# Kernel tuning notes

Hardware: AMD Instinct MI355X
Metric: run time of the kernel (lower is better)

Reference implementation:

```python
import jax, jax.numpy as jnp
import numpy as np

G, P_IN, P_OUT, C_Q = 4, 32, 128, 256
STRIDES = [4, 8, 16, 32]
TAU = 2.0
EPS = 1e-5


def _ln(x, axes):
    m = jnp.mean(x, axes, keepdims=True)
    v = jnp.var(x, axes, keepdims=True)
    return (x - m) * jax.lax.rsqrt(v + EPS)


def _grid_sample(value, pts):
    # torch F.grid_sample, bilinear, padding_mode='zeros', align_corners=False
    # value: [Bg, C, H, W], pts: [Bg, Q, P, 2] in [-1, 1] (x, y order)
    Bg, C, H, W = value.shape
    x = (pts[..., 0] + 1.0) * (W * 0.5) - 0.5
    y = (pts[..., 1] + 1.0) * (H * 0.5) - 0.5
    x0 = jnp.floor(x)
    y0 = jnp.floor(y)
    flat = value.reshape(Bg, C, H * W)
    Q, P = pts.shape[1], pts.shape[2]

    def corner(xf, yf, w):
        valid = (xf >= 0) & (xf <= W - 1) & (yf >= 0) & (yf <= H - 1)
        xi = jnp.clip(xf, 0, W - 1).astype(jnp.int32)
        yi = jnp.clip(yf, 0, H - 1).astype(jnp.int32)
        idx = (yi * W + xi).reshape(Bg, 1, Q * P)
        g = jnp.take_along_axis(flat, idx, axis=2).reshape(Bg, C, Q, P)
        return g * (w * valid)[:, None]

    out = (corner(x0, y0, (x0 + 1 - x) * (y0 + 1 - y))
           + corner(x0 + 1, y0, (x - x0) * (y0 + 1 - y))
           + corner(x0, y0 + 1, (x0 + 1 - x) * (y - y0))
           + corner(x0 + 1, y0 + 1, (x - x0) * (y - y0)))
    return out  # [Bg, C, Q, P]


def setup_inputs() -> dict:
    key = jax.random.key(0)
    ks = jax.random.split(key, 12)
    B, N = 2, 300
    sizes = [(200, 336), (100, 168), (50, 84), (25, 42)]
    xs = [jax.random.normal(ks[i], (B, 256, h, w), jnp.float32) for i, (h, w) in enumerate(sizes)]
    query_feat = jax.random.normal(ks[4], (B, N, C_Q), jnp.float32)
    u = jax.random.uniform(ks[5], (B, N, 4), jnp.float32)
    # xyzr roi: center x in [0,1344], y in [0,800], z (log2 scale) in [3,6], r in [-1,1]
    query_roi = jnp.stack([u[..., 0] * 1344.0, u[..., 1] * 800.0,
                           3.0 + 3.0 * u[..., 2], 2.0 * u[..., 3] - 1.0], axis=-1)
    w_off = jax.random.normal(ks[6], (C_Q, G * P_IN * 3), jnp.float32) * 0.01
    b = jax.random.uniform(ks[7], (G, P_IN, 3), jnp.float32, minval=-0.5, maxval=0.5)
    b_off = b.at[:, :, 2].set(-1.0).reshape(-1)
    cg = 256 // G
    total = G * (cg * cg + P_IN * P_OUT)
    pg_w = jax.random.normal(ks[8], (C_Q, total), jnp.float32) * 0.02
    pg_b = jax.random.normal(ks[9], (total,), jnp.float32) * 0.02
    op_w = jax.random.normal(ks[10], (G * P_OUT * cg, C_Q), jnp.float32) * 0.02
    op_b = jnp.zeros((C_Q,), jnp.float32)
    ln_g = jnp.ones((C_Q,), jnp.float32)
    ln_b = jnp.zeros((C_Q,), jnp.float32)
    return dict(x0=xs[0], x1=xs[1], x2=xs[2], x3=xs[3], query_feat=query_feat,
                query_roi=query_roi, w_off=w_off, b_off=b_off, pg_w=pg_w, pg_b=pg_b,
                op_w=op_w, op_b=op_b, ln_g=ln_g, ln_b=ln_b)


def reference(x0, x1, x2, x3, query_feat, query_roi, w_off, b_off,
              pg_w, pg_b, op_w, op_b, ln_g, ln_b):
    xs = [x0, x1, x2, x3]
    B, N, _ = query_feat.shape
    Cf = x0.shape[1]
    Cg = Cf // G
    L = len(xs)

    # ---- make_sample_points ----
    off = (query_feat @ w_off + b_off).reshape(B, N, G * P_IN, 3)
    xy = query_roi[..., :2]
    z = query_roi[..., 2:3]
    r = query_roi[..., 3:4]
    roi_wh = (2.0 ** z) * jnp.concatenate([2.0 ** (-0.5 * r), 2.0 ** (0.5 * r)], axis=-1)
    samp_xy = xy[:, :, None, :] + off[..., :2] * roi_wh[:, :, None, :]   # [B,N,GP,2]
    samp_lvl = z[:, :, None, :] + off[..., 2:3]                          # [B,N,GP,1]

    # ---- level weights: softmax(-(lvl-3 - l)^2 / tau) ----
    grid = jnp.arange(L, dtype=samp_lvl.dtype)
    lw = jax.nn.softmax(-(((samp_lvl - 3.0) - grid) ** 2) / TAU, axis=-1)  # [B,N,GP,L]

    # ---- multiscale sampling ----
    out = jnp.zeros((B * G, Cg, N, P_IN), x0.dtype)
    for i, (v, s) in enumerate(zip(xs, STRIDES)):
        H, W = v.shape[2], v.shape[3]
        size = jnp.array([W * s, H * s], samp_xy.dtype)
        pts = samp_xy / size * 2.0 - 1.0
        pts = pts.reshape(B, N, G, P_IN, 2).transpose(0, 2, 1, 3, 4).reshape(B * G, N, P_IN, 2)
        val = v.reshape(B * G, Cg, H, W)
        w = lw[..., i].reshape(B, N, G, P_IN).transpose(0, 2, 1, 3).reshape(B * G, 1, N, P_IN)
        out = out + _grid_sample(val, pts) * w
    sampled = out.reshape(B, G, Cg, N, P_IN).transpose(0, 3, 1, 4, 2)  # [B,N,G,P_IN,Cg]

    # ---- AdaptiveMixing ----
    params = (query_feat @ pg_w + pg_b).reshape(B, N, G, -1)
    M = params[..., :Cg * Cg].reshape(B, N, G, Cg, Cg)
    S = params[..., Cg * Cg:].reshape(B, N, G, P_OUT, P_IN)
    h = jnp.einsum('bngpc,bngcd->bngpd', sampled, M)
    h = jax.nn.relu(_ln(h, (-2, -1)))
    h = jnp.einsum('bngop,bngpc->bngoc', S, h)
    h = jax.nn.relu(_ln(h, (-2, -1)))
    q = query_feat + h.reshape(B, N, -1) @ op_w + op_b

    # ---- final LayerNorm (learned) ----
    return _ln(q, (-1,)) * ln_g + ln_b
```

## Files before the change

### kernel.cpp

```cpp
#include <hip/hip_runtime.h>
#include <cstdint>
#include <cstddef>

typedef __bf16 bf16;
typedef _Float16 f16;
typedef __attribute__((ext_vector_type(8))) __bf16 bf16x8;
typedef __attribute__((ext_vector_type(4))) __bf16 bf16x4;
typedef __attribute__((ext_vector_type(4))) float f32x4;
typedef __attribute__((ext_vector_type(2))) float f32x2;
typedef __attribute__((ext_vector_type(2))) uint32_t u32x2;

#define DINL __device__ __forceinline__

DINL float wred(float v) {
#pragma unroll
  for (int m = 32; m; m >>= 1) v += __shfl_xor(v, m, 64);
  return v;
}

DINL int swz(int r) { return ((r ^ (r >> 2)) & 7) << 4; }

__global__ void k_zero(float* __restrict__ p) {
  p[blockIdx.x * 256 + threadIdx.x] = 0.f;
}

__global__ void k_coords(const float* __restrict__ qf, const float* __restrict__ roi,
                         const float* __restrict__ w_off, const float* __restrict__ b_off,
                         float* __restrict__ coords) {
  int bn = blockIdx.x;
  int t = threadIdx.x;
  __shared__ float qs[256];
  __shared__ float offs[384];
  if (t < 256) qs[t] = qf[(size_t)bn * 256 + t];
  __syncthreads();
  float acc = b_off[t];
  for (int k = 0; k < 256; k++) acc += qs[k] * w_off[k * 384 + t];
  offs[t] = acc;
  __syncthreads();
  if (t < 128) {
    float ox = offs[t * 3 + 0], oy = offs[t * 3 + 1], oz = offs[t * 3 + 2];
    float cx = roi[bn * 4 + 0], cy = roi[bn * 4 + 1];
    float z  = roi[bn * 4 + 2], rr = roi[bn * 4 + 3];
    float sx = cx + ox * exp2f(z - 0.5f * rr);
    float sy = cy + oy * exp2f(z + 0.5f * rr);
    float lvl = z + oz;
    float e[4], mx = -1e30f;
#pragma unroll
    for (int l = 0; l < 4; l++) {
      float d = lvl - 3.0f - (float)l;
      e[l] = -d * d * 0.5f;
      mx = fmaxf(mx, e[l]);
    }
    float s = 0.f;
#pragma unroll
    for (int l = 0; l < 4; l++) { e[l] = expf(e[l] - mx); s += e[l]; }
    float inv = 1.f / s;
    float* o = coords + ((size_t)bn * 128 + t) * 6;
    o[0] = sx; o[1] = sy;
#pragma unroll
    for (int l = 0; l < 4; l++) o[2 + l] = e[l] * inv;
  }
}

__global__ __launch_bounds__(256) void k_xpose(
    const float* __restrict__ x0, const float* __restrict__ x1,
    const float* __restrict__ x2, const float* __restrict__ x3,
    f16* __restrict__ xt, int bg0, size_t slab) {
  const int HWl[4]  = {67200, 16800, 4200, 1050};
  const int RB[4]   = {0, 67200, 84000, 88200};
  const float* xs[4] = {x0, x1, x2, x3};
  int bx = blockIdx.x;
  int l, t0;
  if (bx < 525)      { l = 0; t0 = 0; }
  else if (bx < 657) { l = 1; t0 = 525; }
  else if (bx < 690) { l = 2; t0 = 657; }
  else               { l = 3; t0 = 690; }
  int HW = HWl[l];
  int sp0 = (bx - t0) * 128;
  int bg = bg0 + blockIdx.z;
  int b = bg >> 2, g = bg & 3;
  const float* src = xs[l] + (size_t)(b * 256 + g * 64) * HW;
  __shared__ f16 tile[128 * 66];
  int tid = threadIdx.x;
  int lane = tid & 63, wv = tid >> 6;
  int sp = sp0 + lane * 2;
  if (sp < HW) {
#pragma unroll
    for (int j = 0; j < 16; j++) {
      int ch = wv * 16 + j;
      f32x2 v = *(const f32x2*)(src + (size_t)ch * HW + sp);
      tile[(lane * 2 + 0) * 66 + ch] = (f16)v[0];
      tile[(lane * 2 + 1) * 66 + ch] = (f16)v[1];
    }
  }
  __syncthreads();
  f16* dst = xt + slab * blockIdx.z + (size_t)(RB[l] + sp0) * 64;
  int c4 = tid & 15, srow = tid >> 4;
  const uint32_t* tp = (const uint32_t*)(&tile[0]);
#pragma unroll
  for (int it = 0; it < 8; it++) {
    int s = it * 16 + srow;
    if (sp0 + s < HW) {
      u32x2 pk;
      pk[0] = tp[s * 33 + c4 * 2];
      pk[1] = tp[s * 33 + c4 * 2 + 1];
      *(u32x2*)(dst + (size_t)s * 64 + c4 * 4) = pk;
    }
  }
}

__global__ __launch_bounds__(256) void k_sample2(
    const float* __restrict__ coords, const f16* __restrict__ xt,
    bf16* __restrict__ sampled, int bg0, size_t slab) {
  const int   Wl[4] = {336, 168, 84, 42};
  const int   Hl[4] = {200, 100, 50, 25};
  const int   RB[4] = {0, 67200, 84000, 88200};
  const float IS[4] = {0.25f, 0.125f, 0.0625f, 0.03125f};
  int bg = bg0 + blockIdx.z;
  int b = bg >> 2, g = bg & 3;
  int bn = b * 300 + blockIdx.x;
  const f16* xts = xt + slab * blockIdx.z;
  int c = threadIdx.x & 63, pp = threadIdx.x >> 6;
#pragma unroll
  for (int p8i = 0; p8i < 4; p8i++) {
    int p8 = blockIdx.y * 4 + p8i;
    int p = p8 * 4 + pp;
    const float* cd = coords + ((size_t)bn * 128 + g * 32 + p) * 6;
    float sx = cd[0], sy = cd[1];
    float acc = 0.f;
#pragma unroll
    for (int l = 0; l < 4; l++) {
      float wl = cd[2 + l];
      int W = Wl[l], H = Hl[l];
      float xf = sx * IS[l] - 0.5f;
      float yf = sy * IS[l] - 0.5f;
      float xx0 = floorf(xf), yy0 = floorf(yf);
      float fx = xf - xx0, fy = yf - yy0;
      int xi = (int)xx0, yi = (int)yy0;
      const f16* base = xts + (size_t)RB[l] * 64 + c;
      float v = 0.f;
      if (xi >= 0     && xi < W     && yi >= 0     && yi < H)
        v += (1.f - fx) * (1.f - fy) * (float)base[(size_t)(yi * W + xi) * 64];
      if (xi + 1 >= 0 && xi + 1 < W && yi >= 0     && yi < H)
        v += fx * (1.f - fy) * (float)base[(size_t)(yi * W + xi + 1) * 64];
      if (xi >= 0     && xi < W     && yi + 1 >= 0 && yi + 1 < H)
        v += (1.f - fx) * fy * (float)base[(size_t)((yi + 1) * W + xi) * 64];
      if (xi + 1 >= 0 && xi + 1 < W && yi + 1 >= 0 && yi + 1 < H)
        v += fx * fy * (float)base[(size_t)((yi + 1) * W + xi + 1) * 64];
      acc += wl * v;
    }
    sampled[(((size_t)bn * 4 + g) * 32 + p) * 64 + c] = (bf16)acc;
  }
}

__global__ __launch_bounds__(256) void k_params_mfma(
    const float* __restrict__ qf, const float* __restrict__ pg_w,
    const float* __restrict__ pg_b, bf16* __restrict__ pchunk,
    int m_off, int m_cnt) {
  __shared__ char sA[8192];
  __shared__ char sW[32768];
  const int tid = threadIdx.x;
  const int w = tid >> 6, l = tid & 63;
  const int lr = l & 15, lq = l >> 4;
  const int m0 = blockIdx.y * 64;
  const int n0 = blockIdx.x * 256;

  f32x4 acc[4][4];
#pragma unroll
  for (int i = 0; i < 4; i++)
#pragma unroll
    for (int j = 0; j < 4; j++) acc[i][j] = (f32x4)(0.f);

  for (int kt = 0; kt < 4; kt++) {
    const int kb = kt * 64;

#pragma unroll
    for (int i = 0; i < 2; i++) {
      int c = tid * 2 + i;
      int r = c >> 3, kc = c & 7;
      int gm = m0 + r; gm = (gm < m_cnt) ? gm : (m_cnt - 1);
      const float* src = qf + (size_t)(m_off + gm) * 256 + kb + kc * 8;
      f32x4 v0 = *(const f32x4*)src;
      f32x4 v1 = *(const f32x4*)(src + 4);
      bf16x8 t = {(bf16)v0[0], (bf16)v0[1], (bf16)v0[2], (bf16)v0[3],
                  (bf16)v1[0], (bf16)v1[1], (bf16)v1[2], (bf16)v1[3]};
      *(bf16x8*)(sA + r * 128 + ((kc << 4) ^ swz(r))) = t;
    }

#pragma unroll
    for (int i = 0; i < 4; i++) {
      int kblk = i * 4 + w;
      const float* src = pg_w + (size_t)(kb + kblk * 4) * 32768 + n0 + l * 4;
      f32x4 r0 = *(const f32x4*)(src);
      f32x4 r1 = *(const f32x4*)(src + 32768);
      f32x4 r2 = *(const f32x4*)(src + 65536);
      f32x4 r3 = *(const f32x4*)(src + 98304);
      int chv = (kblk >> 1) << 4;
      int sub = (kblk & 1) * 8;
#pragma unroll
      for (int j = 0; j < 4; j++) {
        int n = l * 4 + j;
        bf16x4 t = {(bf16)r0[j], (bf16)r1[j], (bf16)r2[j], (bf16)r3[j]};
        *(bf16x4*)(sW + n * 128 + (chv ^ swz(n)) + sub) = t;
      }
    }
    __syncthreads();

#pragma unroll
    for (int ks = 0; ks < 2; ks++) {
      bf16x8 a[4], b[4];
      int ch = (ks * 4 + lq) << 4;
#pragma unroll
      for (int i = 0; i < 4; i++) {
        int row = i * 16 + lr;
        a[i] = *(const bf16x8*)(sA + row * 128 + (ch ^ swz(row)));
      }
#pragma unroll
      for (int j = 0; j < 4; j++) {
        int nn = w * 64 + j * 16 + lr;
        b[j] = *(const bf16x8*)(sW + nn * 128 + (ch ^ swz(nn)));
      }
#pragma unroll
      for (int i = 0; i < 4; i++)
#pragma unroll
        for (int j = 0; j < 4; j++)
          acc[i][j] = __builtin_amdgcn_mfma_f32_16x16x32_bf16(a[i], b[j], acc[i][j], 0, 0, 0);
    }
    __syncthreads();
  }

#pragma unroll
  for (int i = 0; i < 4; i++) {
#pragma unroll
    for (int r = 0; r < 4; r++) {
      int m = m0 + i * 16 + lq * 4 + r;
      if (m < m_cnt) {
        bf16* dst = pchunk + (size_t)m * 32768 + n0 + w * 64 + lr;
#pragma unroll
        for (int j = 0; j < 4; j++) {
          int n = n0 + w * 64 + j * 16 + lr;
          dst[j * 16] = (bf16)(acc[i][j][r] + pg_b[n]);
        }
      }
    }
  }
}

__global__ __launch_bounds__(256) void k_mix_mfma(
    const bf16* __restrict__ sampled, bf16* __restrict__ params, int m_off) {
  int bnl = blockIdx.x, g = blockIdx.y;
  int tid = threadIdx.x;
  const int w = tid >> 6, l = tid & 63;
  const int lr = l & 15, lq = l >> 4;
  __shared__ char mt[8192];
  __shared__ alignas(16) bf16 h1t[64 * 40];
  __shared__ float red[8];
  const bf16* samp = sampled + ((size_t)(m_off + bnl) * 4 + g) * 2048;
  bf16* pr = params + (size_t)bnl * 32768 + (size_t)g * 8192;

  {
    int cblk = tid >> 4, dblk = tid & 15;
    const bf16* src = pr + cblk * 256 + dblk * 4;
    bf16x4 r0 = *(const bf16x4*)(src);
    bf16x4 r1 = *(const bf16x4*)(src + 64);
    bf16x4 r2 = *(const bf16x4*)(src + 128);
    bf16x4 r3 = *(const bf16x4*)(src + 192);
    int chv = (cblk >> 1) << 4, sub = (cblk & 1) * 8;
#pragma unroll
    for (int j = 0; j < 4; j++) {
      int d = dblk * 4 + j;
      bf16x4 t = {r0[j], r1[j], r2[j], r3[j]};
      *(bf16x4*)(mt + d * 128 + (chv ^ swz(d)) + sub) = t;
    }
  }
  __syncthreads();

  f32x4 acc1[2];
  acc1[0] = (f32x4)(0.f); acc1[1] = (f32x4)(0.f);
  const int dd = w * 16 + lr;
#pragma unroll
  for (int ks = 0; ks < 2; ks++) {
    bf16x8 b = *(const bf16x8*)(mt + dd * 128 + ((((ks << 2) | lq) << 4) ^ swz(dd)));
#pragma unroll
    for (int i = 0; i < 2; i++) {
      bf16x8 a = *(const bf16x8*)(samp + (i * 16 + lr) * 64 + ks * 32 + lq * 8);
      acc1[i] = __builtin_amdgcn_mfma_f32_16x16x32_bf16(a, b, acc1[i], 0, 0, 0);
    }
  }

  {
    float s = 0.f, ss = 0.f;
#pragma unroll
    for (int i = 0; i < 2; i++)
#pragma unroll
      for (int r = 0; r < 4; r++) { float v = acc1[i][r]; s += v; ss += v * v; }
    s = wred(s); ss = wred(ss);
    if (l == 0) { red[w] = s; red[4 + w] = ss; }
    __syncthreads();
    s = red[0] + red[1] + red[2] + red[3];
    ss = red[4] + red[5] + red[6] + red[7];
    float mean = s * (1.f / 2048.f);
    float var = ss * (1.f / 2048.f) - mean * mean;
    float rs = rsqrtf(fmaxf(var, 0.f) + 1e-5f);
#pragma unroll
    for (int i = 0; i < 2; i++)
#pragma unroll
      for (int r = 0; r < 4; r++) {
        float v = (acc1[i][r] - mean) * rs;
        v = v > 0.f ? v : 0.f;
        int p = i * 16 + lq * 4 + r;
        h1t[dd * 40 + p] = (bf16)v;
      }
  }
  __syncthreads();

  f32x4 acc2[2][4];
#pragma unroll
  for (int i = 0; i < 2; i++)
#pragma unroll
    for (int j = 0; j < 4; j++) acc2[i][j] = (f32x4)(0.f);
  bf16x8 b2[4];
#pragma unroll
  for (int j = 0; j < 4; j++)
    b2[j] = *(const bf16x8*)(&h1t[(j * 16 + lr) * 40 + lq * 8]);
#pragma unroll
  for (int i = 0; i < 2; i++) {
    int o = w * 32 + i * 16 + lr;
    bf16x8 a = *(const bf16x8*)(pr + 4096 + o * 32 + lq * 8);
#pragma unroll
    for (int j = 0; j < 4; j++)
      acc2[i][j] = __builtin_amdgcn_mfma_f32_16x16x32_bf16(a, b2[j], acc2[i][j], 0, 0, 0);
  }

  {
    float s = 0.f, ss = 0.f;
#pragma unroll
    for (int i = 0; i < 2; i++)
#pragma unroll
      for (int j = 0; j < 4; j++)
#pragma unroll
        for (int r = 0; r < 4; r++) { float v = acc2[i][j][r]; s += v; ss += v * v; }
    s = wred(s); ss = wred(ss);
    if (l == 0) { red[w] = s; red[4 + w] = ss; }
    __syncthreads();
    s = red[0] + red[1] + red[2] + red[3];
    ss = red[4] + red[5] + red[6] + red[7];
    float mean = s * (1.f / 8192.f);
    float var = ss * (1.f / 8192.f) - mean * mean;
    float rs = rsqrtf(fmaxf(var, 0.f) + 1e-5f);
#pragma unroll
    for (int i = 0; i < 2; i++)
#pragma unroll
      for (int r = 0; r < 4; r++) {
        int o = w * 32 + i * 16 + lq * 4 + r;
#pragma unroll
        for (int j = 0; j < 4; j++) {
          float v = (acc2[i][j][r] - mean) * rs;
          v = v > 0.f ? v : 0.f;
          pr[o * 64 + j * 16 + lr] = (bf16)v;
        }
      }
  }
}

__global__ __launch_bounds__(256) void k_final_mfma(
    const bf16* __restrict__ pchunk, const float* __restrict__ op_w,
    float* __restrict__ facc, int m_off, int m_cnt, int KT) {
  __shared__ char sA[8192];
  __shared__ char sW[32768];
  const int tid = threadIdx.x;
  const int w = tid >> 6, l = tid & 63;
  const int lr = l & 15, lq = l >> 4;
  const int m0 = blockIdx.y * 64;
  const int kb0 = blockIdx.x * (KT * 64);

  f32x4 acc[4][4];
#pragma unroll
  for (int i = 0; i < 4; i++)
#pragma unroll
    for (int j = 0; j < 4; j++) acc[i][j] = (f32x4)(0.f);

  for (int kt = 0; kt < KT; kt++) {
    const int kb = kb0 + kt * 64;

#pragma unroll
    for (int i = 0; i < 2; i++) {
      int c = tid * 2 + i;
      int r = c >> 3, kc = c & 7;
      int gm = m0 + r; gm = (gm < m_cnt) ? gm : (m_cnt - 1);
      f32x4 v = *(const f32x4*)(pchunk + (size_t)gm * 32768 + kb + kc * 8);
      *(f32x4*)(sA + r * 128 + ((kc << 4) ^ swz(r))) = v;
    }

#pragma unroll
    for (int i = 0; i < 4; i++) {
      int kblk = i * 4 + w;
      const float* src = op_w + (size_t)(kb + kblk * 4) * 256 + l * 4;
      f32x4 r0 = *(const f32x4*)(src);
      f32x4 r1 = *(const f32x4*)(src + 256);
      f32x4 r2 = *(const f32x4*)(src + 512);
      f32x4 r3 = *(const f32x4*)(src + 768);
      int chv = (kblk >> 1) << 4;
      int sub = (kblk & 1) * 8;
#pragma unroll
      for (int j = 0; j < 4; j++) {
        int n = l * 4 + j;
        bf16x4 t = {(bf16)r0[j], (bf16)r1[j], (bf16)r2[j], (bf16)r3[j]};
        *(bf16x4*)(sW + n * 128 + (chv ^ swz(n)) + sub) = t;
      }
    }
    __syncthreads();

#pragma unroll
    for (int ks = 0; ks < 2; ks++) {
      bf16x8 a[4], b[4];
      int ch = (ks * 4 + lq) << 4;
#pragma unroll
      for (int i = 0; i < 4; i++) {
        int row = i * 16 + lr;
        a[i] = *(const bf16x8*)(sA + row * 128 + (ch ^ swz(row)));
      }
#pragma unroll
      for (int j = 0; j < 4; j++) {
        int n = w * 64 + j * 16 + lr;
        b[j] = *(const bf16x8*)(sW + n * 128 + (ch ^ swz(n)));
      }
#pragma unroll
      for (int i = 0; i < 4; i++)
#pragma unroll
        for (int j = 0; j < 4; j++)
          acc[i][j] = __builtin_amdgcn_mfma_f32_16x16x32_bf16(a[i], b[j], acc[i][j], 0, 0, 0);
    }
    __syncthreads();
  }

#pragma unroll
  for (int i = 0; i < 4; i++) {
#pragma unroll
    for (int r = 0; r < 4; r++) {
      int m = m0 + i * 16 + lq * 4 + r;
      if (m < m_cnt) {
        float* dst = facc + (size_t)(m_off + m) * 256 + w * 64 + lr;
#pragma unroll
        for (int j = 0; j < 4; j++)
          atomicAdd(dst + j * 16, acc[i][j][r]);
      }
    }
  }
}

__global__ void k_ln(const float* __restrict__ accbuf, const float* __restrict__ qf,
                     const float* __restrict__ opb, const float* __restrict__ lng,
                     const float* __restrict__ lnb, float* __restrict__ out) {
  int bn = blockIdx.x, t = threadIdx.x;
  float v = accbuf[bn * 256 + t] + qf[(size_t)bn * 256 + t] + opb[t];
  __shared__ float red[8];
  float s = wred(v), ss = wred(v * v);
  int w = t >> 6;
  if ((t & 63) == 0) { red[w] = s; red[4 + w] = ss; }
  __syncthreads();
  s = red[0] + red[1] + red[2] + red[3];
  ss = red[4] + red[5] + red[6] + red[7];
  float mean = s * (1.f / 256.f);
  float var = ss * (1.f / 256.f) - mean * mean;
  float y = (v - mean) * rsqrtf(fmaxf(var, 0.f) + 1e-5f);
  out[(size_t)bn * 256 + t] = y * lng[t] + lnb[t];
}

extern "C" void kernel_launch(void* const* d_in, const int* in_sizes, int n_in,
                              void* d_out, int out_size, void* d_ws, size_t ws_size,
                              hipStream_t stream) {
  const float* x0    = (const float*)d_in[0];
  const float* x1    = (const float*)d_in[1];
  const float* x2    = (const float*)d_in[2];
  const float* x3    = (const float*)d_in[3];
  const float* qf    = (const float*)d_in[4];
  const float* roi   = (const float*)d_in[5];
  const float* w_off = (const float*)d_in[6];
  const float* b_off = (const float*)d_in[7];
  const float* pg_w  = (const float*)d_in[8];
  const float* pg_b  = (const float*)d_in[9];
  const float* op_w  = (const float*)d_in[10];
  const float* op_b  = (const float*)d_in[11];
  const float* ln_g  = (const float*)d_in[12];
  const float* ln_b  = (const float*)d_in[13];
  float* out = (float*)d_out;

  const size_t SLAB = 5712000;
  const size_t NEEDED_BIG  = 143001600ull;
  const size_t NEEDED_SMALL = 31948800ull;
  if (ws_size < NEEDED_SMALL) return;

  char* ws = (char*)d_ws;
  float* coords  = (float*)(ws + 0);
  bf16*  sampled = (bf16*)(ws + 1843200);
  float* facc    = (float*)(ws + 11673600);

  k_zero<<<600, 256, 0, stream>>>(facc);
  k_coords<<<600, 384, 0, stream>>>(qf, roi, w_off, b_off, coords);

  if (ws_size >= NEEDED_BIG) {
    bf16* params = (bf16*)(ws + 12288000);
    f16*  xt     = (f16*)(ws + 51609600);
    k_xpose<<<dim3(699, 1, 8), 256, 0, stream>>>(x0, x1, x2, x3, xt, 0, SLAB);
    k_sample2<<<dim3(300, 2, 8), 256, 0, stream>>>(coords, xt, sampled, 0, SLAB);
    k_params_mfma<<<dim3(128, 10), 256, 0, stream>>>(qf, pg_w, pg_b, params, 0, 600);
    k_mix_mfma<<<dim3(600, 4), 256, 0, stream>>>(sampled, params, 0);
    k_final_mfma<<<dim3(64, 10), 256, 0, stream>>>(params, op_w, facc, 0, 600, 8);
  } else {
    bf16* pchunk = (bf16*)(ws + 12288000);
    f16*  xt     = (f16*)(ws + 12288000);
    for (int bg = 0; bg < 8; bg++) {
      k_xpose<<<dim3(699, 1, 1), 256, 0, stream>>>(x0, x1, x2, x3, xt, bg, 0);
      k_sample2<<<dim3(300, 2, 1), 256, 0, stream>>>(coords, xt, sampled, bg, 0);
    }
    for (int chunk = 0; chunk < 2; chunk++) {
      int m_off = chunk * 300, m_cnt = 300;
      k_params_mfma<<<dim3(128, 5), 256, 0, stream>>>(qf, pg_w, pg_b, pchunk, m_off, m_cnt);
      k_mix_mfma<<<dim3(300, 4), 256, 0, stream>>>(sampled, pchunk, m_off);
      k_final_mfma<<<dim3(32, 5), 256, 0, stream>>>(pchunk, op_w, facc, m_off, m_cnt, 16);
    }
  }

  k_ln<<<600, 256, 0, stream>>>(facc, qf, op_b, ln_g, ln_b, out);
}
```

Before: 501.3 us.

## Fuse bilinear multiscale sampling into the adaptive mixing kernel

Removes the separate sampling kernel in the large-workspace path. Each mixing block now gathers its own 32x64 sampled tile straight from the transposed feature maps into swizzled shared memory and feeds it to the MFMA stage. This avoids writing the sampled tensor to global memory, reading it back, and one launch, at the cost of a longer per-block prologue. The transpose kernel also batches its global loads and LDS reads into registers before the stores, to raise memory-level parallelism.

Result: slower. 515.6 us (+2.9%).

```diff
diff --git a/kernel.cpp b/kernel.cpp
--- a/kernel.cpp
+++ b/kernel.cpp
@@ -19,6 +19,7 @@
 }
 
 DINL int swz(int r) { return ((r ^ (r >> 2)) & 7) << 4; }
+DINL int swzc(int r) { return (r ^ (r >> 2)) & 7; }
 
 __global__ void k_zero(float* __restrict__ p) {
   p[blockIdx.x * 256 + threadIdx.x] = 0.f;
@@ -85,26 +86,34 @@
   int lane = tid & 63, wv = tid >> 6;
   int sp = sp0 + lane * 2;
   if (sp < HW) {
+    f32x2 v[16];
+#pragma unroll
+    for (int j = 0; j < 16; j++)
+      v[j] = *(const f32x2*)(src + (size_t)(wv * 16 + j) * HW + sp);
 #pragma unroll
     for (int j = 0; j < 16; j++) {
       int ch = wv * 16 + j;
-      f32x2 v = *(const f32x2*)(src + (size_t)ch * HW + sp);
-      tile[(lane * 2 + 0) * 66 + ch] = (f16)v[0];
-      tile[(lane * 2 + 1) * 66 + ch] = (f16)v[1];
+      tile[(lane * 2 + 0) * 66 + ch] = (f16)v[j][0];
+      tile[(lane * 2 + 1) * 66 + ch] = (f16)v[j][1];
     }
   }
   __syncthreads();
   f16* dst = xt + slab * blockIdx.z + (size_t)(RB[l] + sp0) * 64;
   int c4 = tid & 15, srow = tid >> 4;
   const uint32_t* tp = (const uint32_t*)(&tile[0]);
+  uint32_t pk[16];
+#pragma unroll
+  for (int it = 0; it < 8; it++) {
+    int s = it * 16 + srow;
+    pk[it * 2 + 0] = tp[s * 33 + c4 * 2];
+    pk[it * 2 + 1] = tp[s * 33 + c4 * 2 + 1];
+  }
 #pragma unroll
   for (int it = 0; it < 8; it++) {
     int s = it * 16 + srow;
     if (sp0 + s < HW) {
-      u32x2 pk;
-      pk[0] = tp[s * 33 + c4 * 2];
-      pk[1] = tp[s * 33 + c4 * 2 + 1];
-      *(u32x2*)(dst + (size_t)s * 64 + c4 * 4) = pk;
+      u32x2 q; q[0] = pk[it * 2]; q[1] = pk[it * 2 + 1];
+      *(u32x2*)(dst + (size_t)s * 64 + c4 * 4) = q;
     }
   }
 }
@@ -246,6 +255,162 @@
   }
 }
 
+__global__ __launch_bounds__(256) void k_mix_fused(
+    const float* __restrict__ coords, const f16* __restrict__ xt,
+    bf16* __restrict__ params, size_t slab) {
+  const int   Wl[4] = {336, 168, 84, 42};
+  const int   Hl[4] = {200, 100, 50, 25};
+  const int   RB[4] = {0, 67200, 84000, 88200};
+  const float IS[4] = {0.25f, 0.125f, 0.0625f, 0.03125f};
+  int bn = blockIdx.x, g = blockIdx.y;
+  int b = (bn >= 300) ? 1 : 0;
+  int tid = threadIdx.x;
+  const int w = tid >> 6, l = tid & 63;
+  const int lr = l & 15, lq = l >> 4;
+  __shared__ char mt[8192];
+  __shared__ char samp_s[4096];
+  __shared__ alignas(16) bf16 h1t[64 * 40];
+  __shared__ float red[8];
+  bf16* pr = params + (size_t)bn * 32768 + (size_t)g * 8192;
+  const f16* xts = xt + slab * (size_t)(b * 4 + g);
+
+  {
+    int cblk = tid >> 4, dblk = tid & 15;
+    const bf16* srcm = pr + cblk * 256 + dblk * 4;
+    bf16x4 r0 = *(const bf16x4*)(srcm);
+    bf16x4 r1 = *(const bf16x4*)(srcm + 64);
+    bf16x4 r2 = *(const bf16x4*)(srcm + 128);
+    bf16x4 r3 = *(const bf16x4*)(srcm + 192);
+    int chv = (cblk >> 1) << 4, sub = (cblk & 1) * 8;
+#pragma unroll
+    for (int j = 0; j < 4; j++) {
+      int d = dblk * 4 + j;
+      bf16x4 t = {r0[j], r1[j], r2[j], r3[j]};
+      *(bf16x4*)(mt + d * 128 + (chv ^ swz(d)) + sub) = t;
+    }
+  }
+
+#pragma unroll
+  for (int it = 0; it < 8; it++) {
+    int p = it * 4 + w;
+    const float* cd = coords + ((size_t)bn * 128 + g * 32 + p) * 6;
+    float sx = cd[0], sy = cd[1];
+    float acc = 0.f;
+#pragma unroll
+    for (int lv = 0; lv < 4; lv++) {
+      float wl = cd[2 + lv];
+      int W = Wl[lv], H = Hl[lv];
+      float xf = sx * IS[lv] - 0.5f;
+      float yf = sy * IS[lv] - 0.5f;
+      float xx0 = floorf(xf), yy0 = floorf(yf);
+      float fx = xf - xx0, fy = yf - yy0;
+      int xi = (int)xx0, yi = (int)yy0;
+      const f16* base = xts + (size_t)RB[lv] * 64 + l;
+      float v = 0.f;
+      if (xi >= 0     && xi < W     && yi >= 0     && yi < H)
+        v += (1.f - fx) * (1.f - fy) * (float)base[(size_t)(yi * W + xi) * 64];
+      if (xi + 1 >= 0 && xi + 1 < W && yi >= 0     && yi < H)
+        v += fx * (1.f - fy) * (float)base[(size_t)(yi * W + xi + 1) * 64];
+      if (xi >= 0     && xi < W     && yi + 1 >= 0 && yi + 1 < H)
+        v += (1.f - fx) * fy * (float)base[(size_t)((yi + 1) * W + xi) * 64];
+      if (xi + 1 >= 0 && xi + 1 < W && yi + 1 >= 0 && yi + 1 < H)
+        v += fx * fy * (float)base[(size_t)((yi + 1) * W + xi + 1) * 64];
+      acc += wl * v;
+    }
+    *(bf16*)(samp_s + p * 128 + (((l >> 3) ^ swzc(p)) << 4) + (l & 7) * 2) = (bf16)acc;
+  }
+  __syncthreads();
+
+  f32x4 acc1[2];
+  acc1[0] = (f32x4)(0.f); acc1[1] = (f32x4)(0.f);
+  const int dd = w * 16 + lr;
+#pragma unroll
+  for (int ks = 0; ks < 2; ks++) {
+    bf16x8 bfr = *(const bf16x8*)(mt + dd * 128 + ((((ks << 2) | lq) << 4) ^ swz(dd)));
+#pragma unroll
+    for (int i = 0; i < 2; i++) {
+      int row = i * 16 + lr;
+      bf16x8 a = *(const bf16x8*)(samp_s + row * 128 +
+                                  ((((ks << 2) | lq) ^ swzc(row)) << 4));
+      acc1[i] = __builtin_amdgcn_mfma_f32_16x16x32_bf16(a, bfr, acc1[i], 0, 0, 0);
+    }
+  }
+
+  {
+    float s = 0.f, ss = 0.f;
+#pragma unroll
+    for (int i = 0; i < 2; i++)
+#pragma unroll
+      for (int r = 0; r < 4; r++) { float v = acc1[i][r]; s += v; ss += v * v; }
+    s = wred(s); ss = wred(ss);
+    if (l == 0) { red[w] = s; red[4 + w] = ss; }
+    __syncthreads();
+    s = red[0] + red[1] + red[2] + red[3];
+    ss = red[4] + red[5] + red[6] + red[7];
+    float mean = s * (1.f / 2048.f);
+    float var = ss * (1.f / 2048.f) - mean * mean;
+    float rs = rsqrtf(fmaxf(var, 0.f) + 1e-5f);
+#pragma unroll
+    for (int i = 0; i < 2; i++)
+#pragma unroll
+      for (int r = 0; r < 4; r++) {
+        float v = (acc1[i][r] - mean) * rs;
+        v = v > 0.f ? v : 0.f;
+        int p = i * 16 + lq * 4 + r;
+        h1t[dd * 40 + p] = (bf16)v;
+      }
+  }
+  __syncthreads();
+
+  f32x4 acc2[2][4];
+#pragma unroll
+  for (int i = 0; i < 2; i++)
+#pragma unroll
+    for (int j = 0; j < 4; j++) acc2[i][j] = (f32x4)(0.f);
+  bf16x8 b2[4];
+#pragma unroll
+  for (int j = 0; j < 4; j++)
+    b2[j] = *(const bf16x8*)(&h1t[(j * 16 + lr) * 40 + lq * 8]);
+#pragma unroll
+  for (int i = 0; i < 2; i++) {
+    int o = w * 32 + i * 16 + lr;
+    bf16x8 a = *(const bf16x8*)(pr + 4096 + o * 32 + lq * 8);
+#pragma unroll
+    for (int j = 0; j < 4; j++)
+      acc2[i][j] = __builtin_amdgcn_mfma_f32_16x16x32_bf16(a, b2[j], acc2[i][j], 0, 0, 0);
+  }
+
+  {
+    float s = 0.f, ss = 0.f;
+#pragma unroll
+    for (int i = 0; i < 2; i++)
+#pragma unroll
+      for (int j = 0; j < 4; j++)
+#pragma unroll
+        for (int r = 0; r < 4; r++) { float v = acc2[i][j][r]; s += v; ss += v * v; }
+    s = wred(s); ss = wred(ss);
+    if (l == 0) { red[w] = s; red[4 + w] = ss; }
+    __syncthreads();
+    s = red[0] + red[1] + red[2] + red[3];
+    ss = red[4] + red[5] + red[6] + red[7];
+    float mean = s * (1.f / 8192.f);
+    float var = ss * (1.f / 8192.f) - mean * mean;
+    float rs = rsqrtf(fmaxf(var, 0.f) + 1e-5f);
+#pragma unroll
+    for (int i = 0; i < 2; i++)
+#pragma unroll
+      for (int r = 0; r < 4; r++) {
+        int o = w * 32 + i * 16 + lq * 4 + r;
+#pragma unroll
+        for (int j = 0; j < 4; j++) {
+          float v = (acc2[i][j][r] - mean) * rs;
+          v = v > 0.f ? v : 0.f;
+          pr[o * 64 + j * 16 + lr] = (bf16)v;
+        }
+      }
+  }
+}
+
 __global__ __launch_bounds__(256) void k_mix_mfma(
     const bf16* __restrict__ sampled, bf16* __restrict__ params, int m_off) {
   int bnl = blockIdx.x, g = blockIdx.y;
@@ -280,11 +445,11 @@
   const int dd = w * 16 + lr;
 #pragma unroll
   for (int ks = 0; ks < 2; ks++) {
-    bf16x8 b = *(const bf16x8*)(mt + dd * 128 + ((((ks << 2) | lq) << 4) ^ swz(dd)));
+    bf16x8 bfr = *(const bf16x8*)(mt + dd * 128 + ((((ks << 2) | lq) << 4) ^ swz(dd)));
 #pragma unroll
     for (int i = 0; i < 2; i++) {
       bf16x8 a = *(const bf16x8*)(samp + (i * 16 + lr) * 64 + ks * 32 + lq * 8);
-      acc1[i] = __builtin_amdgcn_mfma_f32_16x16x32_bf16(a, b, acc1[i], 0, 0, 0);
+      acc1[i] = __builtin_amdgcn_mfma_f32_16x16x32_bf16(a, bfr, acc1[i], 0, 0, 0);
     }
   }
 
@@ -503,9 +668,8 @@
     bf16* params = (bf16*)(ws + 12288000);
     f16*  xt     = (f16*)(ws + 51609600);
     k_xpose<<<dim3(699, 1, 8), 256, 0, stream>>>(x0, x1, x2, x3, xt, 0, SLAB);
-    k_sample2<<<dim3(300, 2, 8), 256, 0, stream>>>(coords, xt, sampled, 0, SLAB);
     k_params_mfma<<<dim3(128, 10), 256, 0, stream>>>(qf, pg_w, pg_b, params, 0, 600);
-    k_mix_mfma<<<dim3(600, 4), 256, 0, stream>>>(sampled, params, 0);
+    k_mix_fused<<<dim3(600, 4), 256, 0, stream>>>(coords, xt, params, SLAB);
     k_final_mfma<<<dim3(64, 10), 256, 0, stream>>>(params, op_w, facc, 0, 600, 8);
   } else {
     bf16* pchunk = (bf16*)(ws + 12288000);
```
